# Kernel tuning notes

Measured on AMD Instinct MI355X. Metric: run time of the kernel, lower is better.

The kernel has to match this reference:

```python
import jax, jax.numpy as jnp
import numpy as np
from jax import lax

B, T, K = 16, 8, 64
COUT, CIN, KH, KW = 128, 128, 5, 5
H, W = 64, 64
PAD = 2  # p=2 in batch_conv -> same spatial size for 5x5


def setup_inputs() -> dict:
    key = jax.random.key(0)
    k1, k2, k3 = jax.random.split(key, 3)
    x = jax.random.normal(k1, (B, CIN, H, W), dtype=jnp.float32)
    task_features = jax.random.normal(k2, (B, T, K), dtype=jnp.float32)
    # learned weight bank (kaiming-uniform in torch; scaled normal is fine for a reference)
    fan_in = CIN * KH * KW
    weights = jax.random.normal(k3, (K, COUT, CIN, KH, KW), dtype=jnp.float32) / np.sqrt(fan_in)
    return {"x": x, "task_features": task_features, "weights": weights}


def reference(x, task_features, weights):
    # infer_params: per-demonstration weighted sum over the K weight bank,
    # then mean over demonstrations T. Fused into one contraction:
    #   sum_t sum_k tf[b,t,k] * W[k,o,c,i,j] / T
    layer_params = jnp.einsum('btk,kocij->bocij', task_features, weights) / T  # (B,Cout,Cin,kh,kw)

    # batch_conv: per-example conv2d with padding 2 (group=B pattern)
    def conv_one(xi, wi):
        # xi: (Cin,H,W), wi: (Cout,Cin,kh,kw)
        return lax.conv_general_dilated(
            xi[None], wi, window_strides=(1, 1),
            padding=[(PAD, PAD), (PAD, PAD)],
            dimension_numbers=('NCHW', 'OIHW', 'NCHW'))[0]

    y = jax.vmap(conv_one)(x, layer_params)  # (B, Cout, H, W)
    return y
```

## Files before the change

kernel.cpp:

```cpp
#include <hip/hip_runtime.h>

#define B_    16
#define T_    8
#define K_    64
#define COUT  128
#define CIN   128
#define H_    64
#define W_    64
#define WSZ   (COUT*CIN*5*5)

typedef __bf16 bf16x8 __attribute__((ext_vector_type(8)));
typedef float  f32x4  __attribute__((ext_vector_type(4)));

static __device__ __forceinline__ unsigned short f2bf(float f) {
    unsigned int u = __builtin_bit_cast(unsigned int, f);
    unsigned int r = (u + 0x7FFFu + ((u >> 16) & 1u)) >> 16;
    return (unsigned short)r;
}

static __device__ __forceinline__ unsigned int pack2(float lo, float hi) {
    return (unsigned int)f2bf(lo) | ((unsigned int)f2bf(hi) << 16);
}

__global__ __launch_bounds__(256) void prep_kernel(const float* __restrict__ Wb,
                                                   const float* __restrict__ tf,
                                                   const float* __restrict__ x,
                                                   unsigned short* __restrict__ lpF,
                                                   unsigned short* __restrict__ xT) {
    __shared__ __align__(16) char smem[30720];
    int tid = threadIdx.x;

    if (blockIdx.x < 512) {
        float* cs          = (float*)smem;
        unsigned short* lt = (unsigned short*)(smem + 4096);

        int o = blockIdx.x >> 2;
        int s = blockIdx.x & 3;

        {
            int idx = tid;
#pragma unroll
            for (int r = 0; r < 4; ++r, idx += 256) {
                int b = idx >> 6, k = idx & 63;
                float sum = 0.f;
#pragma unroll
                for (int t = 0; t < T_; ++t) sum += tf[(b * T_ + t) * K_ + k];
                cs[idx] = sum * 0.125f;
            }
        }
        __syncthreads();

        if (tid < 200) {
            int base = o * 3200 + s * 800 + tid * 4;
            float4 acc[B_];
#pragma unroll
            for (int b = 0; b < B_; ++b) acc[b] = make_float4(0.f, 0.f, 0.f, 0.f);

#pragma unroll 4
            for (int k = 0; k < K_; ++k) {
                const float4 wv = *(const float4*)(Wb + (size_t)k * WSZ + base);
#pragma unroll
                for (int b = 0; b < B_; ++b) {
                    float c = cs[b * K_ + k];
                    acc[b].x += c * wv.x;
                    acc[b].y += c * wv.y;
                    acc[b].z += c * wv.z;
                    acc[b].w += c * wv.w;
                }
            }
            unsigned int* ltw = (unsigned int*)lt;
#pragma unroll
            for (int b = 0; b < B_; ++b) {
                ltw[b * 400 + tid * 2]     = pack2(acc[b].x, acc[b].y);
                ltw[b * 400 + tid * 2 + 1] = pack2(acc[b].z, acc[b].w);
            }
        }
        __syncthreads();

        int wm = o >> 6, mt = (o >> 4) & 3, n16 = o & 15;
        for (int it = tid; it < 1600; it += 256) {
            int b = it / 100;
            int r = it - b * 100;
            int tap = r >> 2;
            int quad = r & 3;
            unsigned short v[8];
#pragma unroll
            for (int j = 0; j < 8; ++j)
                v[j] = lt[b * 800 + (quad * 8 + j) * 25 + tap];
            size_t off = (size_t)b * 409600
                       + (size_t)((((tap * 4 + s) * 2 + wm) * 4 + mt) * 512
                                  + quad * 128 + n16 * 8);
            *(uint4*)(lpF + off) = *(const uint4*)v;
        }
    } else {
        unsigned short* ls = (unsigned short*)smem;
        int q = blockIdx.x - 512;
        int b = q >> 6, h = q & 63;

        int w = tid & 63, cb = tid >> 6;
        const float* xp = x + (((size_t)(b * CIN + cb * 32) * H_ + h) * W_) + w;
#pragma unroll
        for (int p = 0; p < 16; ++p) {
            float f0 = xp[(size_t)(2 * p) * (H_ * W_)];
            float f1 = xp[(size_t)(2 * p + 1) * (H_ * W_)];
            *(unsigned int*)&ls[w * 136 + cb * 32 + 2 * p] = pack2(f0, f1);
        }
        __syncthreads();

        unsigned short* xTb = xT + ((size_t)(b * 64 + h) * 64) * 128;
        int chunk = tid & 15, wr = tid >> 4;
#pragma unroll
        for (int pass = 0; pass < 4; ++pass) {
            int ww = pass * 16 + wr;
            uint4 v = *(const uint4*)&ls[ww * 136 + chunk * 8];
            *(uint4*)&xTb[ww * 128 + chunk * 8] = v;
        }
    }
}

__global__ __launch_bounds__(256) void conv_mfma(const unsigned short* __restrict__ xT,
                                                 const unsigned short* __restrict__ lpF,
                                                 float* __restrict__ out) {
    int bid = blockIdx.x;
    int b  = (bid & 7) | (((bid >> 3) & 1) << 3);
    int h0 = (bid >> 4) << 1;

    int tid  = threadIdx.x;
    int lane = tid & 63, wq = tid >> 6;
    int n16 = lane & 15, quad = lane >> 4;

    __shared__ __align__(16) unsigned short xs[408 * 40];

    f32x4 acc[2][8];
#pragma unroll
    for (int mt = 0; mt < 2; ++mt)
#pragma unroll
        for (int nt = 0; nt < 8; ++nt) acc[mt][nt] = (f32x4){0.f, 0.f, 0.f, 0.f};

    const unsigned short* xTb = xT + (size_t)b * (64 * 64 * 128);
    const unsigned short* lpW = lpF + (size_t)b * 409600
                              + (wq >> 1) * 2048 + (wq & 1) * 1024 + lane * 8;

#define LOAD_FRAGS(A, Bf, tap) do {                                          \
    int i_ = (tap) / 5, j_ = (tap) - 5 * (i_);                               \
    const unsigned short* ap_ = lpW + (tap) * 16384 + kcB;                   \
    A[0] = *(const bf16x8*)(ap_);                                            \
    A[1] = *(const bf16x8*)(ap_ + 512);                                      \
    const unsigned short* bp_ = &xs[((i_) * 68 + n16 + j_) * 40 + quad * 8]; \
    Bf[0] = *(const bf16x8*)(bp_);                                           \
    Bf[1] = *(const bf16x8*)(bp_ + 16 * 40);                                 \
    Bf[2] = *(const bf16x8*)(bp_ + 32 * 40);                                 \
    Bf[3] = *(const bf16x8*)(bp_ + 48 * 40);                                 \
    Bf[4] = *(const bf16x8*)(bp_ + 68 * 40);                                 \
    Bf[5] = *(const bf16x8*)(bp_ + (68 + 16) * 40);                          \
    Bf[6] = *(const bf16x8*)(bp_ + (68 + 32) * 40);                          \
    Bf[7] = *(const bf16x8*)(bp_ + (68 + 48) * 40);                          \
} while (0)

#define DO_MFMA(av, bv) do {                                                 \
    _Pragma("unroll") for (int mt = 0; mt < 2; ++mt)                         \
    _Pragma("unroll") for (int nt = 0; nt < 8; ++nt)                         \
        acc[mt][nt] = __builtin_amdgcn_mfma_f32_16x16x32_bf16(               \
            (av)[mt], (bv)[nt], acc[mt][nt], 0, 0, 0);                       \
} while (0)

    for (int kc = 0; kc < 4; ++kc) {
        int kcOff = kc * 32;
        int kcB   = kc * 4096;
        __syncthreads();
        for (int sIdx = tid; sIdx < 408; sIdx += 256) {
            unsigned int su = (unsigned int)sIdx;
            int rr = su / 68u;
            int ww = su - rr * 68u;
            int gr = h0 - 2 + rr, gw = ww - 2;
            uint4* dst = (uint4*)&xs[sIdx * 40];
            if ((unsigned)gr < 64u && (unsigned)gw < 64u) {
                const uint4* src = (const uint4*)(xTb + (((size_t)gr * 64 + gw) * 128 + kcOff));
                dst[0] = src[0]; dst[1] = src[1]; dst[2] = src[2]; dst[3] = src[3];
            } else {
                uint4 z = {0u, 0u, 0u, 0u};
                dst[0] = z; dst[1] = z; dst[2] = z; dst[3] = z;
            }
        }
        __syncthreads();

        bf16x8 a0[2], b0[8], a1[2], b1[8];
        LOAD_FRAGS(a0, b0, 0);
        for (int t = 0; t < 24; t += 2) {
            LOAD_FRAGS(a1, b1, t + 1);
            DO_MFMA(a0, b0);
            LOAD_FRAGS(a0, b0, t + 2);
            DO_MFMA(a1, b1);
        }
        DO_MFMA(a0, b0);
    }

    float* outb = out + (size_t)b * (COUT * H_ * W_);
#pragma unroll
    for (int mt = 0; mt < 2; ++mt) {
#pragma unroll
        for (int nt = 0; nt < 8; ++nt) {
#pragma unroll
            for (int r = 0; r < 4; ++r) {
                int o = wq * 32 + mt * 16 + quad * 4 + r;
                int h = h0 + (nt >> 2);
                int w = (nt & 3) * 16 + n16;
                outb[(size_t)o * (H_ * W_) + (size_t)h * W_ + w] = acc[mt][nt][r];
            }
        }
    }
#undef LOAD_FRAGS
#undef DO_MFMA
}

extern "C" void kernel_launch(void* const* d_in, const int* in_sizes, int n_in,
                              void* d_out, int out_size, void* d_ws, size_t ws_size,
                              hipStream_t stream) {
    const float* x  = (const float*)d_in[0];
    const float* tf = (const float*)d_in[1];
    const float* Wb = (const float*)d_in[2];
    float* out = (float*)d_out;

    unsigned short* lpF = (unsigned short*)d_ws;
    unsigned short* xT  = lpF + (size_t)B_ * 409600;

    prep_kernel<<<1536, 256, 0, stream>>>(Wb, tf, x, lpF, xT);
    conv_mfma  <<<512,  256, 0, stream>>>(xT, lpF, out);
}
```

Before: 239.5 us.

## Stream weight-bank loads through an LDS ring with async global_load_lds prefetch

The weight-mixing phase of the prep kernel now issues direct global-to-LDS loads into an 8-deep ring buffer, prefetching eight K-slices ahead and waiting on vmcnt before each use. The coefficient table is transposed to k-major so the 16 per-batch coefficients come in as four float4 LDS reads instead of 16 scalar reads. The aim is to hide the global load latency of the 64 strided weight reads per thread. In exchange it relies on manual waitcnt and sched_barrier control, uses more shared memory, and has every wave issue loads including the idle lanes, whose offsets are clamped to zero.

```diff
diff --git a/kernel.cpp b/kernel.cpp
--- a/kernel.cpp
+++ b/kernel.cpp
@@ -11,6 +11,7 @@
 
 typedef __bf16 bf16x8 __attribute__((ext_vector_type(8)));
 typedef float  f32x4  __attribute__((ext_vector_type(4)));
+typedef unsigned int u32;
 
 static __device__ __forceinline__ unsigned short f2bf(float f) {
     unsigned int u = __builtin_bit_cast(unsigned int, f);
@@ -20,6 +21,12 @@
 
 static __device__ __forceinline__ unsigned int pack2(float lo, float hi) {
     return (unsigned int)f2bf(lo) | ((unsigned int)f2bf(hi) << 16);
+}
+
+static __device__ __forceinline__ void stage16(const void* g, void* l) {
+    __builtin_amdgcn_global_load_lds((const __attribute__((address_space(1))) u32*)g,
+                                     (__attribute__((address_space(3))) u32*)l,
+                                     16, 0, 0);
 }
 
 __global__ __launch_bounds__(256) void prep_kernel(const float* __restrict__ Wb,
@@ -27,11 +34,11 @@
                                                    const float* __restrict__ x,
                                                    unsigned short* __restrict__ lpF,
                                                    unsigned short* __restrict__ xT) {
-    __shared__ __align__(16) char smem[30720];
+    __shared__ __align__(16) char smem[36864];
     int tid = threadIdx.x;
 
     if (blockIdx.x < 512) {
-        float* cs          = (float*)smem;
+        float* cs2         = (float*)smem;
         unsigned short* lt = (unsigned short*)(smem + 4096);
 
         int o = blockIdx.x >> 2;
@@ -41,33 +48,85 @@
             int idx = tid;
 #pragma unroll
             for (int r = 0; r < 4; ++r, idx += 256) {
-                int b = idx >> 6, k = idx & 63;
+                int k = idx >> 4, b = idx & 15;
                 float sum = 0.f;
 #pragma unroll
                 for (int t = 0; t < T_; ++t) sum += tf[(b * T_ + t) * K_ + k];
-                cs[idx] = sum * 0.125f;
-            }
-        }
+                cs2[idx] = sum * 0.125f;
+            }
+        }
+        __syncthreads();
+
+        int wv_ = tid >> 6;
+        int ln_ = tid & 63;
+        int so  = 256 * wv_ + 4 * ln_;
+        if (so >= 800) so = 0;
+        const float* gbase = Wb + o * 3200 + s * 800 + so;
+        char* ring = smem + 4096;
+        char* mydst = ring + wv_ * 1024;
+
+#pragma unroll
+        for (int u = 0; u < 8; ++u)
+            stage16(gbase + (size_t)u * WSZ, mydst + u * 4096);
+
+        float4 acc[B_];
+#pragma unroll
+        for (int b = 0; b < B_; ++b) acc[b] = make_float4(0.f, 0.f, 0.f, 0.f);
+
+        const char* myrd = ring + tid * 16;
+
+        for (int k = 0; k < 64; ++k) {
+            int slot = k & 7;
+            asm volatile("s_waitcnt vmcnt(7)" ::: "memory");
+            float4 wvv, c0, c1, c2, c3;
+            if (tid < 200) {
+                wvv = *(const float4*)(myrd + slot * 4096);
+                const float4* cp = (const float4*)(cs2 + k * 16);
+                c0 = cp[0]; c1 = cp[1]; c2 = cp[2]; c3 = cp[3];
+            }
+            asm volatile("s_waitcnt lgkmcnt(0)" ::: "memory");
+            __builtin_amdgcn_sched_barrier(0);
+            stage16(gbase + (size_t)((k + 8) & 63) * WSZ, mydst + slot * 4096);
+            if (tid < 200) {
+                acc[0].x  += c0.x * wvv.x; acc[0].y  += c0.x * wvv.y;
+                acc[0].z  += c0.x * wvv.z; acc[0].w  += c0.x * wvv.w;
+                acc[1].x  += c0.y * wvv.x; acc[1].y  += c0.y * wvv.y;
+                acc[1].z  += c0.y * wvv.z; acc[1].w  += c0.y * wvv.w;
+                acc[2].x  += c0.z * wvv.x; acc[2].y  += c0.z * wvv.y;
+                acc[2].z  += c0.z * wvv.z; acc[2].w  += c0.z * wvv.w;
+                acc[3].x  += c0.w * wvv.x; acc[3].y  += c0.w * wvv.y;
+                acc[3].z  += c0.w * wvv.z; acc[3].w  += c0.w * wvv.w;
+                acc[4].x  += c1.x * wvv.x; acc[4].y  += c1.x * wvv.y;
+                acc[4].z  += c1.x * wvv.z; acc[4].w  += c1.x * wvv.w;
+                acc[5].x  += c1.y * wvv.x; acc[5].y  += c1.y * wvv.y;
+                acc[5].z  += c1.y * wvv.z; acc[5].w  += c1.y * wvv.w;
+                acc[6].x  += c1.z * wvv.x; acc[6].y  += c1.z * wvv.y;
+                acc[6].z  += c1.z * wvv.z; acc[6].w  += c1.z * wvv.w;
+                acc[7].x  += c1.w * wvv.x; acc[7].y  += c1.w * wvv.y;
+                acc[7].z  += c1.w * wvv.z; acc[7].w  += c1.w * wvv.w;
+                acc[8].x  += c2.x * wvv.x; acc[8].y  += c2.x * wvv.y;
+                acc[8].z  += c2.x * wvv.z; acc[8].w  += c2.x * wvv.w;
+                acc[9].x  += c2.y * wvv.x; acc[9].y  += c2.y * wvv.y;
+                acc[9].z  += c2.y * wvv.z; acc[9].w  += c2.y * wvv.w;
+                acc[10].x += c2.z * wvv.x; acc[10].y += c2.z * wvv.y;
+                acc[10].z += c2.z * wvv.z; acc[10].w += c2.z * wvv.w;
+                acc[11].x += c2.w * wvv.x; acc[11].y += c2.w * wvv.y;
+                acc[11].z += c2.w * wvv.z; acc[11].w += c2.w * wvv.w;
+                acc[12].x += c3.x * wvv.x; acc[12].y += c3.x * wvv.y;
+                acc[12].z += c3.x * wvv.z; acc[12].w += c3.x * wvv.w;
+                acc[13].x += c3.y * wvv.x; acc[13].y += c3.y * wvv.y;
+                acc[13].z += c3.y * wvv.z; acc[13].w += c3.y * wvv.w;
+                acc[14].x += c3.z * wvv.x; acc[14].y += c3.z * wvv.y;
+                acc[14].z += c3.z * wvv.z; acc[14].w += c3.z * wvv.w;
+                acc[15].x += c3.w * wvv.x; acc[15].y += c3.w * wvv.y;
+                acc[15].z += c3.w * wvv.z; acc[15].w += c3.w * wvv.w;
+            }
+        }
+
+        asm volatile("s_waitcnt vmcnt(0)" ::: "memory");
         __syncthreads();
 
         if (tid < 200) {
-            int base = o * 3200 + s * 800 + tid * 4;
-            float4 acc[B_];
-#pragma unroll
-            for (int b = 0; b < B_; ++b) acc[b] = make_float4(0.f, 0.f, 0.f, 0.f);
-
-#pragma unroll 4
-            for (int k = 0; k < K_; ++k) {
-                const float4 wv = *(const float4*)(Wb + (size_t)k * WSZ + base);
-#pragma unroll
-                for (int b = 0; b < B_; ++b) {
-                    float c = cs[b * K_ + k];
-                    acc[b].x += c * wv.x;
-                    acc[b].y += c * wv.y;
-                    acc[b].z += c * wv.z;
-                    acc[b].w += c * wv.w;
-                }
-            }
             unsigned int* ltw = (unsigned int*)lt;
 #pragma unroll
             for (int b = 0; b < B_; ++b) {
```

Measured after the change: 254.4 us. 6.2% more time.

## Double-buffer weight-bank loads via global_load_lds and split batch across half-blocks

Applied to the files above, without the earlier changes.

Rewrites the weight-combination part of the prep kernel so 256 threads stage the weight-bank slices straight into a double-buffered LDS ring with global_load_lds. The other threads compute from the current buffer, while each half of a 512-thread block handles eight batch entries. The x-transpose blocks are interleaved with the weight blocks and each now handles two rows. The aim is to hide global-load latency and raise occupancy in the memory-bound prep stage. In exchange it relies on hand-placed waitcnt and barriers, which are fragile, and it uses more shared memory per block.

```diff
diff --git a/kernel.cpp b/kernel.cpp
--- a/kernel.cpp
+++ b/kernel.cpp
@@ -11,6 +11,7 @@
 
 typedef __bf16 bf16x8 __attribute__((ext_vector_type(8)));
 typedef float  f32x4  __attribute__((ext_vector_type(4)));
+typedef unsigned int u32;
 
 static __device__ __forceinline__ unsigned short f2bf(float f) {
     unsigned int u = __builtin_bit_cast(unsigned int, f);
@@ -22,63 +23,123 @@
     return (unsigned int)f2bf(lo) | ((unsigned int)f2bf(hi) << 16);
 }
 
-__global__ __launch_bounds__(256) void prep_kernel(const float* __restrict__ Wb,
-                                                   const float* __restrict__ tf,
-                                                   const float* __restrict__ x,
-                                                   unsigned short* __restrict__ lpF,
-                                                   unsigned short* __restrict__ xT) {
-    __shared__ __align__(16) char smem[30720];
+static __device__ __forceinline__ void stage16(const void* g, void* l) {
+    __builtin_amdgcn_global_load_lds((const __attribute__((address_space(1))) u32*)g,
+                                     (__attribute__((address_space(3))) u32*)l,
+                                     16, 0, 0);
+}
+
+__global__ __launch_bounds__(512, 4) void prep_kernel(const float* __restrict__ Wb,
+                                                      const float* __restrict__ tf,
+                                                      const float* __restrict__ x,
+                                                      unsigned short* __restrict__ lpF,
+                                                      unsigned short* __restrict__ xT) {
+    __shared__ __align__(16) char smem[36864];
     int tid = threadIdx.x;
 
-    if (blockIdx.x < 512) {
-        float* cs          = (float*)smem;
+    if ((blockIdx.x & 1) == 0) {
+        float* cs2         = (float*)smem;
+        char*  ring        = smem + 4096;
         unsigned short* lt = (unsigned short*)(smem + 4096);
 
-        int o = blockIdx.x >> 2;
-        int s = blockIdx.x & 3;
+        int chunk = blockIdx.x >> 1;
+        int o = chunk >> 2;
+        int s = chunk & 3;
 
         {
             int idx = tid;
 #pragma unroll
-            for (int r = 0; r < 4; ++r, idx += 256) {
-                int b = idx >> 6, k = idx & 63;
+            for (int r = 0; r < 2; ++r, idx += 512) {
+                int k = idx >> 4, b = idx & 15;
                 float sum = 0.f;
 #pragma unroll
                 for (int t = 0; t < T_; ++t) sum += tf[(b * T_ + t) * K_ + k];
-                cs[idx] = sum * 0.125f;
-            }
-        }
-        __syncthreads();
-
-        if (tid < 200) {
-            int base = o * 3200 + s * 800 + tid * 4;
-            float4 acc[B_];
-#pragma unroll
-            for (int b = 0; b < B_; ++b) acc[b] = make_float4(0.f, 0.f, 0.f, 0.f);
-
-#pragma unroll 4
-            for (int k = 0; k < K_; ++k) {
-                const float4 wv = *(const float4*)(Wb + (size_t)k * WSZ + base);
-#pragma unroll
-                for (int b = 0; b < B_; ++b) {
-                    float c = cs[b * K_ + k];
-                    acc[b].x += c * wv.x;
-                    acc[b].y += c * wv.y;
-                    acc[b].z += c * wv.z;
-                    acc[b].w += c * wv.w;
+                cs2[idx] = sum * 0.125f;
+            }
+        }
+        __syncthreads();
+
+        int w_   = (tid >> 6) & 3;
+        bool stager = tid < 256;
+        int ln_  = tid & 63;
+        int cln  = ln_ < 50 ? ln_ : 49;
+        const float* wp = Wb + o * 3200 + s * 800 + w_ * 200 + cln * 4;
+
+        int u    = tid & 255;
+        int half = tid >> 8;
+        int myoff = ((u / 50) << 10) + (u % 50) * 16;
+        bool cons = u < 200;
+
+        float4 acc[8];
+#pragma unroll
+        for (int b = 0; b < 8; ++b) acc[b] = make_float4(0.f, 0.f, 0.f, 0.f);
+
+        if (stager) {
+#pragma unroll
+            for (int kk = 0; kk < 4; ++kk)
+                stage16(wp + (size_t)kk * WSZ, ring + kk * 4096 + w_ * 1024);
+        }
+
+#pragma unroll 2
+        for (int g = 0; g < 16; ++g) {
+            int buf = g & 1;
+            char* curb = ring + buf * 16384;
+            char* nxtb = ring + (buf ^ 1) * 16384;
+            if (stager) {
+                int kn = ((g + 1) * 4) & 63;
+#pragma unroll
+                for (int kk = 0; kk < 4; ++kk)
+                    stage16(wp + (size_t)(kn + kk) * WSZ, nxtb + kk * 4096 + w_ * 1024);
+            }
+            asm volatile("s_waitcnt vmcnt(4)" ::: "memory");
+            __builtin_amdgcn_s_barrier();
+            __builtin_amdgcn_sched_barrier(0);
+            if (cons) {
+#pragma unroll
+                for (int kk = 0; kk < 4; ++kk) {
+                    int k = g * 4 + kk;
+                    float4 wv = *(const float4*)(curb + kk * 4096 + myoff);
+                    const float4* cp = (const float4*)(cs2 + k * 16 + half * 8);
+                    float4 c0 = cp[0], c1 = cp[1];
+                    acc[0].x += c0.x * wv.x; acc[0].y += c0.x * wv.y;
+                    acc[0].z += c0.x * wv.z; acc[0].w += c0.x * wv.w;
+                    acc[1].x += c0.y * wv.x; acc[1].y += c0.y * wv.y;
+                    acc[1].z += c0.y * wv.z; acc[1].w += c0.y * wv.w;
+                    acc[2].x += c0.z * wv.x; acc[2].y += c0.z * wv.y;
+                    acc[2].z += c0.z * wv.z; acc[2].w += c0.z * wv.w;
+                    acc[3].x += c0.w * wv.x; acc[3].y += c0.w * wv.y;
+                    acc[3].z += c0.w * wv.z; acc[3].w += c0.w * wv.w;
+                    acc[4].x += c1.x * wv.x; acc[4].y += c1.x * wv.y;
+                    acc[4].z += c1.x * wv.z; acc[4].w += c1.x * wv.w;
+                    acc[5].x += c1.y * wv.x; acc[5].y += c1.y * wv.y;
+                    acc[5].z += c1.y * wv.z; acc[5].w += c1.y * wv.w;
+                    acc[6].x += c1.z * wv.x; acc[6].y += c1.z * wv.y;
+                    acc[6].z += c1.z * wv.z; acc[6].w += c1.z * wv.w;
+                    acc[7].x += c1.w * wv.x; acc[7].y += c1.w * wv.y;
+                    acc[7].z += c1.w * wv.z; acc[7].w += c1.w * wv.w;
                 }
             }
+            asm volatile("s_waitcnt lgkmcnt(0)" ::: "memory");
+            __builtin_amdgcn_sched_barrier(0);
+            __builtin_amdgcn_s_barrier();
+        }
+
+        asm volatile("s_waitcnt vmcnt(0)" ::: "memory");
+        __syncthreads();
+
+        if (cons) {
             unsigned int* ltw = (unsigned int*)lt;
 #pragma unroll
-            for (int b = 0; b < B_; ++b) {
-                ltw[b * 400 + tid * 2]     = pack2(acc[b].x, acc[b].y);
-                ltw[b * 400 + tid * 2 + 1] = pack2(acc[b].z, acc[b].w);
+            for (int lb = 0; lb < 8; ++lb) {
+                int b = half * 8 + lb;
+                ltw[b * 400 + u * 2]     = pack2(acc[lb].x, acc[lb].y);
+                ltw[b * 400 + u * 2 + 1] = pack2(acc[lb].z, acc[lb].w);
             }
         }
         __syncthreads();
 
         int wm = o >> 6, mt = (o >> 4) & 3, n16 = o & 15;
-        for (int it = tid; it < 1600; it += 256) {
+        for (int it = tid; it < 1600; it += 512) {
             int b = it / 100;
             int r = it - b * 100;
             int tap = r >> 2;
@@ -93,11 +154,13 @@
             *(uint4*)(lpF + off) = *(const uint4*)v;
         }
     } else {
-        unsigned short* ls = (unsigned short*)smem;
-        int q = blockIdx.x - 512;
+        int h2 = tid >> 8;
+        int t2 = tid & 255;
+        unsigned short* ls = (unsigned short*)(smem + h2 * 17408);
+        int q = (blockIdx.x >> 1) * 2 + h2;
         int b = q >> 6, h = q & 63;
 
-        int w = tid & 63, cb = tid >> 6;
+        int w = t2 & 63, cb = t2 >> 6;
         const float* xp = x + (((size_t)(b * CIN + cb * 32) * H_ + h) * W_) + w;
 #pragma unroll
         for (int p = 0; p < 16; ++p) {
@@ -108,7 +171,7 @@
         __syncthreads();
 
         unsigned short* xTb = xT + ((size_t)(b * 64 + h) * 64) * 128;
-        int chunk = tid & 15, wr = tid >> 4;
+        int chunk = t2 & 15, wr = t2 >> 4;
 #pragma unroll
         for (int pass = 0; pass < 4; ++pass) {
             int ww = pass * 16 + wr;
@@ -224,6 +287,6 @@
     unsigned short* lpF = (unsigned short*)d_ws;
     unsigned short* xT  = lpF + (size_t)B_ * 409600;
 
-    prep_kernel<<<1536, 256, 0, stream>>>(Wb, tf, x, lpF, xT);
+    prep_kernel<<<1024, 512, 0, stream>>>(Wb, tf, x, lpF, xT);
     conv_mfma  <<<512,  256, 0, stream>>>(xT, lpF, out);
 }
```

Measured after the change: 252.6 us. 1.05x slower.
